# Kernel tuning notes

Hardware: AMD Instinct MI355X
Metric: run time of the kernel (lower is better)

## Reference

```python
import jax, jax.numpy as jnp
import numpy as np

SEQ_LEN = 1024
BATCH = 256
HIDDEN = 100
OUT = 1

L_FILTER = [-0.0106, 0.0329, 0.0308, -0.187, -0.028, 0.6309, 0.7148, 0.2304]
H_FILTER = [-0.2304, 0.7148, -0.6309, -0.028, 0.187, 0.0308, -0.0329, -0.0106]


def _create_W(P, is_l, rng):
    filt = L_FILTER if is_l else H_FILTER
    eps = np.min(np.abs(filt))
    W = rng.standard_normal((P, P)) * 0.1 * eps
    for i in range(P):
        for k, j in enumerate(range(i, min(i + len(filt), P))):
            W[i, j] = filt[k]
    return jnp.asarray(W, dtype=jnp.float32)


def setup_inputs() -> dict:
    key = jax.random.key(0)
    ks = jax.random.split(key, 16)
    rng = np.random.default_rng(0)
    T, H = SEQ_LEN, HIDDEN
    s = 1.0 / np.sqrt(H)

    def lstm_params(k):
        k1, k2, k3 = jax.random.split(k, 3)
        Wih = jax.random.uniform(k1, (4 * H, 1), jnp.float32, -s, s)
        Whh = jax.random.uniform(k2, (4 * H, H), jnp.float32, -s, s)
        b = jax.random.uniform(k3, (4 * H,), jnp.float32, -s, s)
        return Wih, Whh, b

    Wih1, Whh1, b1 = lstm_params(ks[0])
    Wih2, Whh2, b2 = lstm_params(ks[1])
    Wih3, Whh3, b3 = lstm_params(ks[2])
    return {
        "x": jax.random.normal(ks[3], (BATCH, T, 1), jnp.float32),
        "W1H": _create_W(T, False, rng),
        "b1H": jax.random.uniform(ks[4], (T,), jnp.float32, -1 / np.sqrt(T), 1 / np.sqrt(T)),
        "W1L": _create_W(T, True, rng),
        "b1L": jax.random.uniform(ks[5], (T,), jnp.float32, -1 / np.sqrt(T), 1 / np.sqrt(T)),
        "W2H": _create_W(T // 2, False, rng),
        "b2H": jax.random.uniform(ks[6], (T // 2,), jnp.float32, -1 / np.sqrt(T // 2), 1 / np.sqrt(T // 2)),
        "W2L": _create_W(T // 2, True, rng),
        "b2L": jax.random.uniform(ks[7], (T // 2,), jnp.float32, -1 / np.sqrt(T // 2), 1 / np.sqrt(T // 2)),
        "Wih1": Wih1, "Whh1": Whh1, "b1": b1,
        "Wih2": Wih2, "Whh2": Whh2, "b2": b2,
        "Wih3": Wih3, "Whh3": Whh3, "b3": b3,
        "Wout": jax.random.uniform(ks[8], (OUT, H), jnp.float32, -s, s),
        "bout": jax.random.uniform(ks[9], (OUT,), jnp.float32, -s, s),
    }


def _avgpool2(x):  # [B, L] -> [B, L//2], AvgPool1d(kernel=2, stride=2)
    B, L = x.shape
    return x.reshape(B, L // 2, 2).mean(-1)


def _lstm(x, Wih, Whh, b):
    # x: [B, T, 1]; torch LSTM gate order i, f, g, o; h0 = c0 = 0
    H = Whh.shape[1]
    gx = jnp.einsum('bti,gi->btg', x, Wih) + b  # [B, T, 4H]

    def step(carry, g):
        h, c = carry
        z = g + h @ Whh.T
        i, f, gg, o = jnp.split(z, 4, axis=-1)
        c = jax.nn.sigmoid(f) * c + jax.nn.sigmoid(i) * jnp.tanh(gg)
        h = jax.nn.sigmoid(o) * jnp.tanh(c)
        return (h, c), h

    B = x.shape[0]
    h0 = jnp.zeros((B, H), x.dtype)
    _, hs = jax.lax.scan(step, (h0, h0), jnp.swapaxes(gx, 0, 1))
    return jnp.swapaxes(hs, 0, 1)  # [B, T, H]


def reference(x, W1H, b1H, W1L, b1L, W2H, b2H, W2L, b2L,
              Wih1, Whh1, b1, Wih2, Whh2, b2, Wih3, Whh3, b3, Wout, bout):
    inp = x[:, :, -1]  # [B, T]
    ah1 = jax.nn.sigmoid(inp @ W1H.T + b1H)
    al1 = jax.nn.sigmoid(inp @ W1L.T + b1L)
    xh1 = _avgpool2(ah1)  # [B, T/2]
    xl1 = _avgpool2(al1)  # [B, T/2]
    ah2 = jax.nn.sigmoid(xl1 @ W2H.T + b2H)
    al2 = jax.nn.sigmoid(xl1 @ W2L.T + b2L)
    xh2 = _avgpool2(ah2)  # [B, T/4]
    xl2 = _avgpool2(al2)  # [B, T/4]
    s1 = _lstm(xh1[..., None], Wih1, Whh1, b1)
    s2 = _lstm(xh2[..., None], Wih2, Whh2, b2)
    s3 = _lstm(xl2[..., None], Wih3, Whh3, b3)
    cat = jnp.concatenate([s1, s2, s3], axis=1)  # [B, T, H]
    out = cat @ Wout.T + bout  # [B, T, OUT]
    return out[:, -1, :]
```

## Files before the change

kernel.cpp:

```cpp
#include <hip/hip_runtime.h>
#include <math.h>

typedef __bf16 bf16x8 __attribute__((ext_vector_type(8)));
typedef float f32x4 __attribute__((ext_vector_type(4)));

__device__ __forceinline__ unsigned short f2bf(float f) {
  unsigned int u = __builtin_bit_cast(unsigned int, f);
  u += 0x7fffu + ((u >> 16) & 1u);
  return (unsigned short)(u >> 16);
}
__device__ __forceinline__ unsigned int pack2bf(float a, float b) {
  return (unsigned int)f2bf(a) | ((unsigned int)f2bf(b) << 16);
}

#define GK_PADK 40
template <int WFP32, int XFP32>
__global__ __launch_bounds__(256) void gemm_mfma_sig_pool(
    const void* __restrict__ Wv, const float* __restrict__ bias,
    const void* __restrict__ Xv, void* __restrict__ Y,
    int K, int Np, int out_bf16) {
  __shared__ unsigned short Wt[64][GK_PADK];
  __shared__ unsigned short Xt[64][GK_PADK];
  const int tid = threadIdx.x;
  const int i_base = blockIdx.x * 64;
  const int b_base = blockIdx.y * 64;
  const int srow = tid >> 2, sseg = tid & 3;
  const int wv = tid >> 6, lane = tid & 63;
  const int wn = wv & 1, wb = wv >> 1;
  const int L15 = lane & 15, q = lane >> 4;

  f32x4 acc[2][2] = {};
  for (int k0 = 0; k0 < K; k0 += 32) {
    if (WFP32) {
      const float* Wf = (const float*)Wv;
      const float4 a = *(const float4*)&Wf[(size_t)(i_base + srow) * K + k0 + sseg * 8];
      const float4 b = *(const float4*)&Wf[(size_t)(i_base + srow) * K + k0 + sseg * 8 + 4];
      uint4 p = { pack2bf(a.x, a.y), pack2bf(a.z, a.w), pack2bf(b.x, b.y), pack2bf(b.z, b.w) };
      *(uint4*)&Wt[srow][sseg * 8] = p;
    } else {
      *(uint4*)&Wt[srow][sseg * 8] =
          *(const uint4*)&((const unsigned short*)Wv)[(size_t)(i_base + srow) * K + k0 + sseg * 8];
    }
    if (XFP32) {
      const float* Xf = (const float*)Xv;
      const float4 a = *(const float4*)&Xf[(size_t)(b_base + srow) * K + k0 + sseg * 8];
      const float4 b = *(const float4*)&Xf[(size_t)(b_base + srow) * K + k0 + sseg * 8 + 4];
      uint4 p = { pack2bf(a.x, a.y), pack2bf(a.z, a.w), pack2bf(b.x, b.y), pack2bf(b.z, b.w) };
      *(uint4*)&Xt[srow][sseg * 8] = p;
    } else {
      *(uint4*)&Xt[srow][sseg * 8] =
          *(const uint4*)&((const unsigned short*)Xv)[(size_t)(b_base + srow) * K + k0 + sseg * 8];
    }
    __syncthreads();
    bf16x8 a0 = *(const bf16x8*)&Wt[wn * 32 + L15][q * 8];
    bf16x8 a1 = *(const bf16x8*)&Wt[wn * 32 + 16 + L15][q * 8];
    bf16x8 b0 = *(const bf16x8*)&Xt[wb * 32 + L15][q * 8];
    bf16x8 b1 = *(const bf16x8*)&Xt[wb * 32 + 16 + L15][q * 8];
    acc[0][0] = __builtin_amdgcn_mfma_f32_16x16x32_bf16(a0, b0, acc[0][0], 0, 0, 0);
    acc[0][1] = __builtin_amdgcn_mfma_f32_16x16x32_bf16(a0, b1, acc[0][1], 0, 0, 0);
    acc[1][0] = __builtin_amdgcn_mfma_f32_16x16x32_bf16(a1, b0, acc[1][0], 0, 0, 0);
    acc[1][1] = __builtin_amdgcn_mfma_f32_16x16x32_bf16(a1, b1, acc[1][1], 0, 0, 0);
    __syncthreads();
  }

  const int nb0 = i_base + wn * 32;
  const int bc0 = b_base + wb * 32 + L15;
#pragma unroll
  for (int mg = 0; mg < 2; mg++) {
    const int nrow = nb0 + mg * 16 + q * 4;
    const float bi0 = bias[nrow], bi1 = bias[nrow + 1];
    const float bi2 = bias[nrow + 2], bi3 = bias[nrow + 3];
#pragma unroll
    for (int bg = 0; bg < 2; bg++) {
      const int b = bc0 + bg * 16;
      f32x4 A = acc[mg][bg];
      const float a0 = __builtin_amdgcn_rcpf(1.f + __expf(-(A[0] + bi0)));
      const float a1 = __builtin_amdgcn_rcpf(1.f + __expf(-(A[1] + bi1)));
      const float a2 = __builtin_amdgcn_rcpf(1.f + __expf(-(A[2] + bi2)));
      const float a3 = __builtin_amdgcn_rcpf(1.f + __expf(-(A[3] + bi3)));
      const float p0 = 0.5f * (a0 + a1), p1 = 0.5f * (a2 + a3);
      const int pidx = nrow >> 1;
      if (out_bf16) {
        *(unsigned int*)&((unsigned short*)Y)[(size_t)b * Np + pidx] = pack2bf(p0, p1);
      } else {
        *(float2*)&((float*)Y)[(size_t)b * Np + pidx] = make_float2(p0, p1);
      }
    }
  }
}

#define HID 100
#define TSTEPS 256

__device__ __forceinline__ float qx1(float x) {
  int v = __builtin_amdgcn_mov_dpp(__builtin_bit_cast(int, x), 0xB1, 0xf, 0xf, true);
  return x + __builtin_bit_cast(float, v);
}
__device__ __forceinline__ float qx2(float x) {
  int v = __builtin_amdgcn_mov_dpp(__builtin_bit_cast(int, x), 0x4E, 0xf, 0xf, true);
  return x + __builtin_bit_cast(float, v);
}

__global__ __launch_bounds__(448) __attribute__((amdgpu_waves_per_eu(1, 2)))
void lstm_tail(
    const float* __restrict__ X, const float* __restrict__ Wih,
    const float* __restrict__ Whh, const float* __restrict__ bg,
    const float* __restrict__ Wout, const float* __restrict__ bout,
    float* __restrict__ out) {
  const int bat = blockIdx.x;
  const int t = threadIdx.x;
  const int r = t >> 2;
  const int kq = t & 3;
  const int koff = 25 * kq;
  const bool valid = (r < HID);
  const int rr = valid ? r : 0;
  __shared__ __align__(16) float hbuf[2][128];
  __shared__ float xrow[TSTEPS];
  __shared__ float red[HID];

  for (int i = t; i < TSTEPS; i += 448) xrow[i] = X[(size_t)bat * TSTEPS + i];

  const float* Wr0 = &Whh[(size_t)(0 * HID + rr) * HID + koff];
  const float* Wr1 = &Whh[(size_t)(1 * HID + rr) * HID + koff];
  const float* Wr2 = &Whh[(size_t)(2 * HID + rr) * HID + koff];
  const float* Wr3 = &Whh[(size_t)(3 * HID + rr) * HID + koff];

#define DECLW(P) float4 P##_0, P##_1, P##_2, P##_3, P##_4, P##_5; float P##_6;
  DECLW(wi) DECLW(wf) DECLW(wg) DECLW(wo)
#undef DECLW
#define LW(P, B)                                      \
  P##_0 = make_float4(B[0],  B[1],  B[2],  B[3]);     \
  P##_1 = make_float4(B[4],  B[5],  B[6],  B[7]);     \
  P##_2 = make_float4(B[8],  B[9],  B[10], B[11]);    \
  P##_3 = make_float4(B[12], B[13], B[14], B[15]);    \
  P##_4 = make_float4(B[16], B[17], B[18], B[19]);    \
  P##_5 = make_float4(B[20], B[21], B[22], B[23]);    \
  P##_6 = B[24];
  LW(wi, Wr0) LW(wf, Wr1) LW(wg, Wr2) LW(wo, Wr3)
#undef LW

  const float bi_ = bg[0 * HID + rr], bf_ = bg[1 * HID + rr];
  const float bg_ = bg[2 * HID + rr], bo_ = bg[3 * HID + rr];
  const float ui = Wih[0 * HID + rr], uf = Wih[1 * HID + rr];
  const float ug = Wih[2 * HID + rr], uo = Wih[3 * HID + rr];

  const int hpos = ((rr / 25) << 5) + (rr % 25);

  if (t < 128) { hbuf[0][t] = 0.f; hbuf[1][t] = 0.f; }
  float c = 0.f;
  __syncthreads();

  for (int step = 0; step < TSTEPS; step++) {
    const float* hq = &hbuf[step & 1][kq << 5];
    float z0 = 0.f, z1 = 0.f, z2 = 0.f, z3 = 0.f;
#define G4(OFF, WI, WF, WG, WO)                                                  \
    { const float4 h4 = *(const float4*)&hq[OFF];                                \
      z0 = fmaf(WI.x, h4.x, z0); z1 = fmaf(WF.x, h4.x, z1);                      \
      z2 = fmaf(WG.x, h4.x, z2); z3 = fmaf(WO.x, h4.x, z3);                      \
      z0 = fmaf(WI.y, h4.y, z0); z1 = fmaf(WF.y, h4.y, z1);                      \
      z2 = fmaf(WG.y, h4.y, z2); z3 = fmaf(WO.y, h4.y, z3);                      \
      z0 = fmaf(WI.z, h4.z, z0); z1 = fmaf(WF.z, h4.z, z1);                      \
      z2 = fmaf(WG.z, h4.z, z2); z3 = fmaf(WO.z, h4.z, z3);                      \
      z0 = fmaf(WI.w, h4.w, z0); z1 = fmaf(WF.w, h4.w, z1);                      \
      z2 = fmaf(WG.w, h4.w, z2); z3 = fmaf(WO.w, h4.w, z3); }
    G4(0,  wi_0, wf_0, wg_0, wo_0)
    G4(4,  wi_1, wf_1, wg_1, wo_1)
    G4(8,  wi_2, wf_2, wg_2, wo_2)
    G4(12, wi_3, wf_3, wg_3, wo_3)
    G4(16, wi_4, wf_4, wg_4, wo_4)
    G4(20, wi_5, wf_5, wg_5, wo_5)
    { const float h1 = hq[24];
      z0 = fmaf(wi_6, h1, z0); z1 = fmaf(wf_6, h1, z1);
      z2 = fmaf(wg_6, h1, z2); z3 = fmaf(wo_6, h1, z3); }
#undef G4
    z0 = qx2(qx1(z0)); z1 = qx2(qx1(z1)); z2 = qx2(qx1(z2)); z3 = qx2(qx1(z3));

    const float xt = xrow[step];
    const float zi = fmaf(ui, xt, z0 + bi_);
    const float zf = fmaf(uf, xt, z1 + bf_);
    const float zg = fmaf(ug, xt, z2 + bg_);
    const float zo = fmaf(uo, xt, z3 + bo_);
    const float ai = __builtin_amdgcn_rcpf(1.f + __expf(-zi));
    const float af = __builtin_amdgcn_rcpf(1.f + __expf(-zf));
    const float ag = 2.f * __builtin_amdgcn_rcpf(1.f + __expf(-2.f * zg)) - 1.f;
    const float ao = __builtin_amdgcn_rcpf(1.f + __expf(-zo));
    c = fmaf(af, c, ai * ag);
    const float th = 2.f * __builtin_amdgcn_rcpf(1.f + __expf(-2.f * c)) - 1.f;
    if (kq == 0 && valid) hbuf[(step & 1) ^ 1][hpos] = ao * th;
    __syncthreads();
  }

  if (t < HID) {
    const int mc = t / 25, mr2 = t % 25;
    red[t] = hbuf[0][(mc << 5) + mr2] * Wout[t];
  }
  __syncthreads();
  if (t == 0) {
    float s = 0.f;
#pragma unroll
    for (int k = 0; k < HID; k++) s += red[k];
    out[bat] = s + bout[0];
  }
}

extern "C" void kernel_launch(void* const* d_in, const int* in_sizes, int n_in,
                              void* d_out, int out_size, void* d_ws, size_t ws_size,
                              hipStream_t stream) {
  const float* x    = (const float*)d_in[0];
  const float* W1L  = (const float*)d_in[3];
  const float* b1L  = (const float*)d_in[4];
  const float* W2L  = (const float*)d_in[7];
  const float* b2L  = (const float*)d_in[8];
  const float* Wih3 = (const float*)d_in[15];
  const float* Whh3 = (const float*)d_in[16];
  const float* b3   = (const float*)d_in[17];
  const float* Wout = (const float*)d_in[18];
  const float* bout = (const float*)d_in[19];
  float* out = (float*)d_out;

  unsigned short* xl1b = (unsigned short*)d_ws;
  float* xl2 = (float*)(xl1b + (size_t)256 * 512);

  gemm_mfma_sig_pool<1, 1><<<dim3(16, 4), 256, 0, stream>>>(W1L, b1L, x, xl1b, 1024, 512, 1);
  gemm_mfma_sig_pool<1, 0><<<dim3(8, 4), 256, 0, stream>>>(W2L, b2L, xl1b, xl2, 512, 256, 0);
  lstm_tail<<<256, 448, 0, stream>>>(xl2, Wih3, Whh3, b3, Wout, bout, out);
}
```

Baseline: 281.7 us.

## Split LSTM gate rows across twice the threads with a shared gate buffer

Each LSTM block now uses 832 threads. Each thread holds two gate rows instead of four, which halves its per-step FMA chain and weight register footprint. Gate activations are written to a shared buffer, and 100 threads then combine them into the cell and hidden state. The price is a second __syncthreads per timestep and an extra shared-memory round trip in a latency-bound serial loop.

```diff
diff --git a/kernel.cpp b/kernel.cpp
--- a/kernel.cpp
+++ b/kernel.cpp
@@ -91,6 +91,8 @@
 
 #define HID 100
 #define TSTEPS 256
+#define LTHREADS 832
+#define HSTRIDE 36
 
 __device__ __forceinline__ float qx1(float x) {
   int v = __builtin_amdgcn_mov_dpp(__builtin_bit_cast(int, x), 0xB1, 0xf, 0xf, true);
@@ -101,32 +103,34 @@
   return x + __builtin_bit_cast(float, v);
 }
 
-__global__ __launch_bounds__(448) __attribute__((amdgpu_waves_per_eu(1, 2)))
+__global__ __launch_bounds__(LTHREADS) __attribute__((amdgpu_waves_per_eu(1, 4)))
 void lstm_tail(
     const float* __restrict__ X, const float* __restrict__ Wih,
-    const float* __restrict__ Whh, const float* __restrict__ bg,
+    const float* __restrict__ Whh, const float* __restrict__ bgates,
     const float* __restrict__ Wout, const float* __restrict__ bout,
     float* __restrict__ out) {
   const int bat = blockIdx.x;
   const int t = threadIdx.x;
-  const int r = t >> 2;
+  const int r = t >> 3;
+  const int gp = (t >> 2) & 1;
   const int kq = t & 3;
+  const bool wvalid = (r < HID);
+  const int rr = wvalid ? r : 0;
+  const int rowA = gp * 200 + rr;
+  const int rowB = rowA + 100;
   const int koff = 25 * kq;
-  const bool valid = (r < HID);
-  const int rr = valid ? r : 0;
-  __shared__ __align__(16) float hbuf[2][128];
+
+  __shared__ __align__(16) float hbuf[2][160];
+  __shared__ float zs[400];
   __shared__ float xrow[TSTEPS];
   __shared__ float red[HID];
 
-  for (int i = t; i < TSTEPS; i += 448) xrow[i] = X[(size_t)bat * TSTEPS + i];
-
-  const float* Wr0 = &Whh[(size_t)(0 * HID + rr) * HID + koff];
-  const float* Wr1 = &Whh[(size_t)(1 * HID + rr) * HID + koff];
-  const float* Wr2 = &Whh[(size_t)(2 * HID + rr) * HID + koff];
-  const float* Wr3 = &Whh[(size_t)(3 * HID + rr) * HID + koff];
-
+  for (int i = t; i < TSTEPS; i += LTHREADS) xrow[i] = X[(size_t)bat * TSTEPS + i];
+
+  const float* WA = &Whh[(size_t)rowA * HID + koff];
+  const float* WB = &Whh[(size_t)rowB * HID + koff];
 #define DECLW(P) float4 P##_0, P##_1, P##_2, P##_3, P##_4, P##_5; float P##_6;
-  DECLW(wi) DECLW(wf) DECLW(wg) DECLW(wo)
+  DECLW(wa) DECLW(wb)
 #undef DECLW
 #define LW(P, B)                                      \
   P##_0 = make_float4(B[0],  B[1],  B[2],  B[3]);     \
@@ -136,64 +140,59 @@
   P##_4 = make_float4(B[16], B[17], B[18], B[19]);    \
   P##_5 = make_float4(B[20], B[21], B[22], B[23]);    \
   P##_6 = B[24];
-  LW(wi, Wr0) LW(wf, Wr1) LW(wg, Wr2) LW(wo, Wr3)
+  LW(wa, WA) LW(wb, WB)
 #undef LW
 
-  const float bi_ = bg[0 * HID + rr], bf_ = bg[1 * HID + rr];
-  const float bg_ = bg[2 * HID + rr], bo_ = bg[3 * HID + rr];
-  const float ui = Wih[0 * HID + rr], uf = Wih[1 * HID + rr];
-  const float ug = Wih[2 * HID + rr], uo = Wih[3 * HID + rr];
-
-  const int hpos = ((rr / 25) << 5) + (rr % 25);
-
-  if (t < 128) { hbuf[0][t] = 0.f; hbuf[1][t] = 0.f; }
+  const bool doact = wvalid && (kq == 1 || kq == 2);
+  const int wrow = (kq == 1) ? rowA : rowB;
+  const float u_  = Wih[wrow];
+  const float bz_ = bgates[wrow];
+  const bool is_tanh = (kq == 1 && gp == 1);
+  const float ka = is_tanh ? 2.f : 1.f;
+  const float ma = is_tanh ? 2.f : 1.f;
+  const float da = is_tanh ? -1.f : 0.f;
+
+  if (t < 160) { hbuf[0][t] = 0.f; hbuf[1][t] = 0.f; }
   float c = 0.f;
   __syncthreads();
 
   for (int step = 0; step < TSTEPS; step++) {
-    const float* hq = &hbuf[step & 1][kq << 5];
-    float z0 = 0.f, z1 = 0.f, z2 = 0.f, z3 = 0.f;
-#define G4(OFF, WI, WF, WG, WO)                                                  \
-    { const float4 h4 = *(const float4*)&hq[OFF];                                \
-      z0 = fmaf(WI.x, h4.x, z0); z1 = fmaf(WF.x, h4.x, z1);                      \
-      z2 = fmaf(WG.x, h4.x, z2); z3 = fmaf(WO.x, h4.x, z3);                      \
-      z0 = fmaf(WI.y, h4.y, z0); z1 = fmaf(WF.y, h4.y, z1);                      \
-      z2 = fmaf(WG.y, h4.y, z2); z3 = fmaf(WO.y, h4.y, z3);                      \
-      z0 = fmaf(WI.z, h4.z, z0); z1 = fmaf(WF.z, h4.z, z1);                      \
-      z2 = fmaf(WG.z, h4.z, z2); z3 = fmaf(WO.z, h4.z, z3);                      \
-      z0 = fmaf(WI.w, h4.w, z0); z1 = fmaf(WF.w, h4.w, z1);                      \
-      z2 = fmaf(WG.w, h4.w, z2); z3 = fmaf(WO.w, h4.w, z3); }
-    G4(0,  wi_0, wf_0, wg_0, wo_0)
-    G4(4,  wi_1, wf_1, wg_1, wo_1)
-    G4(8,  wi_2, wf_2, wg_2, wo_2)
-    G4(12, wi_3, wf_3, wg_3, wo_3)
-    G4(16, wi_4, wf_4, wg_4, wo_4)
-    G4(20, wi_5, wf_5, wg_5, wo_5)
+    const int cur = step & 1;
+    const float* hq = &hbuf[cur][kq * HSTRIDE];
+    float za = 0.f, zb = 0.f;
+#define DG(OFF, A, B)                                        \
+    { const float4 h4 = *(const float4*)&hq[OFF];            \
+      za = fmaf(A.x, h4.x, za); zb = fmaf(B.x, h4.x, zb);    \
+      za = fmaf(A.y, h4.y, za); zb = fmaf(B.y, h4.y, zb);    \
+      za = fmaf(A.z, h4.z, za); zb = fmaf(B.z, h4.z, zb);    \
+      za = fmaf(A.w, h4.w, za); zb = fmaf(B.w, h4.w, zb); }
+    DG(0,  wa_0, wb_0)
+    DG(4,  wa_1, wb_1)
+    DG(8,  wa_2, wb_2)
+    DG(12, wa_3, wb_3)
+    DG(16, wa_4, wb_4)
+    DG(20, wa_5, wb_5)
     { const float h1 = hq[24];
-      z0 = fmaf(wi_6, h1, z0); z1 = fmaf(wf_6, h1, z1);
-      z2 = fmaf(wg_6, h1, z2); z3 = fmaf(wo_6, h1, z3); }
-#undef G4
-    z0 = qx2(qx1(z0)); z1 = qx2(qx1(z1)); z2 = qx2(qx1(z2)); z3 = qx2(qx1(z3));
-
-    const float xt = xrow[step];
-    const float zi = fmaf(ui, xt, z0 + bi_);
-    const float zf = fmaf(uf, xt, z1 + bf_);
-    const float zg = fmaf(ug, xt, z2 + bg_);
-    const float zo = fmaf(uo, xt, z3 + bo_);
-    const float ai = __builtin_amdgcn_rcpf(1.f + __expf(-zi));
-    const float af = __builtin_amdgcn_rcpf(1.f + __expf(-zf));
-    const float ag = 2.f * __builtin_amdgcn_rcpf(1.f + __expf(-2.f * zg)) - 1.f;
-    const float ao = __builtin_amdgcn_rcpf(1.f + __expf(-zo));
-    c = fmaf(af, c, ai * ag);
-    const float th = 2.f * __builtin_amdgcn_rcpf(1.f + __expf(-2.f * c)) - 1.f;
-    if (kq == 0 && valid) hbuf[(step & 1) ^ 1][hpos] = ao * th;
-    __syncthreads();
-  }
-
-  if (t < HID) {
-    const int mc = t / 25, mr2 = t % 25;
-    red[t] = hbuf[0][(mc << 5) + mr2] * Wout[t];
-  }
+      za = fmaf(wa_6, h1, za); zb = fmaf(wb_6, h1, zb); }
+#undef DG
+    za = qx2(qx1(za));
+    zb = qx2(qx1(zb));
+    if (doact) {
+      const float zsel = (kq == 1) ? za : zb;
+      const float zfull = fmaf(u_, xrow[step], zsel + bz_);
+      zs[wrow] = ma * __builtin_amdgcn_rcpf(1.f + __expf(-ka * zfull)) + da;
+    }
+    __syncthreads();
+    if (t < HID) {
+      const float ai = zs[t], af = zs[t + 100], ag = zs[t + 200], ao = zs[t + 300];
+      c = fmaf(af, c, ai * ag);
+      const float th = 2.f * __builtin_amdgcn_rcpf(1.f + __expf(-2.f * c)) - 1.f;
+      hbuf[cur ^ 1][(t / 25) * HSTRIDE + (t % 25)] = ao * th;
+    }
+    __syncthreads();
+  }
+
+  if (t < HID) red[t] = hbuf[0][(t / 25) * HSTRIDE + (t % 25)] * Wout[t];
   __syncthreads();
   if (t == 0) {
     float s = 0.f;
@@ -223,5 +222,5 @@
 
   gemm_mfma_sig_pool<1, 1><<<dim3(16, 4), 256, 0, stream>>>(W1L, b1L, x, xl1b, 1024, 512, 1);
   gemm_mfma_sig_pool<1, 0><<<dim3(8, 4), 256, 0, stream>>>(W2L, b2L, xl1b, xl2, 512, 256, 0);
-  lstm_tail<<<256, 448, 0, stream>>>(xl2, Wih3, Whh3, b3, Wout, bout, out);
-}
+  lstm_tail<<<256, LTHREADS, 0, stream>>>(xl2, Wih3, Whh3, b3, Wout, bout, out);
+}
```

Result: no change. 286.6 us (+1.8%).
